# Kernel tuning notes

Hardware: AMD Instinct MI355X
Metric: run time of the kernel (lower is better)

Reference implementation:

```python
import jax, jax.numpy as jnp
import numpy as np

N_NODES = 100000
N_EDGES = 1600000
NODE_DIM = 128
EDGE_DIM = 64
MSG_DIM = 128
NODE_DIM_OUT = 128


def setup_inputs() -> dict:
    key = jax.random.key(0)
    k1, k2, k3, k4, k5, k6, k7 = jax.random.split(key, 7)
    node_emb = jax.random.normal(k1, (N_NODES, NODE_DIM), dtype=jnp.float32)
    edge_index = jax.random.randint(k2, (2, N_EDGES), 0, N_NODES, dtype=jnp.int64)
    edge_emb = jax.random.normal(k3, (N_EDGES, EDGE_DIM), dtype=jnp.float32)
    # Linear params (stored as [in, out]; torch uses [out, in] with x @ W.T)
    s_msg = 1.0 / np.sqrt(NODE_DIM + EDGE_DIM)
    W_msg = jax.random.uniform(k4, (NODE_DIM + EDGE_DIM, MSG_DIM), jnp.float32, -s_msg, s_msg)
    b_msg = jax.random.uniform(k5, (MSG_DIM,), jnp.float32, -s_msg, s_msg)
    s_upd = 1.0 / np.sqrt(NODE_DIM + MSG_DIM)
    W_upd = jax.random.uniform(k6, (NODE_DIM + MSG_DIM, NODE_DIM_OUT), jnp.float32, -s_upd, s_upd)
    b_upd = jax.random.uniform(k7, (NODE_DIM_OUT,), jnp.float32, -s_upd, s_upd)
    return {"node_emb": node_emb, "edge_index": edge_index, "edge_emb": edge_emb,
            "W_msg": W_msg, "b_msg": b_msg, "W_upd": W_upd, "b_upd": b_upd}


def reference(node_emb, edge_index, edge_emb, W_msg, b_msg, W_upd, b_upd):
    # PyG MessagePassing default flow: x_j = x[edge_index[0]] (source),
    # messages aggregated (mean) at edge_index[1] (target).
    src = edge_index[0]
    dst = edge_index[1]
    n = node_emb.shape[0]

    x_j = node_emb[src]                                    # [E, node_dim] gather
    msg_in = jnp.concatenate([x_j, edge_emb], axis=1)      # [E, node_dim+edge_dim]
    msg = jax.nn.relu(msg_in @ W_msg + b_msg)              # [E, msg_dim]

    # scatter-mean aggregate to nodes
    summed = jax.ops.segment_sum(msg, dst, num_segments=n)  # [N, msg_dim]
    counts = jax.ops.segment_sum(jnp.ones((msg.shape[0],), dtype=msg.dtype), dst, num_segments=n)
    mean_msg = summed / jnp.maximum(counts, 1.0)[:, None]

    upd_in = jnp.concatenate([node_emb, mean_msg], axis=1)  # [N, node_dim+msg_dim]
    h = jax.nn.relu(upd_in @ W_upd + b_upd)                 # [N, node_dim_out]
    # dropout is identity in eval mode; normalize=False (default)
    return h
```

## Files before the change

### kernel.cpp

```cpp
#include <hip/hip_runtime.h>
#include <hip/hip_bf16.h>

#define N_NODES 100000
#define N_EDGES 1600000
#define D_NODE 128
#define D_EDGE 64
#define D_MSG 128
#define K1 192
#define K2 256
#define D_OUT 128
#define NSB 98
#define TILE 64
#define NT (N_EDGES / TILE)

using frag8 = __attribute__((ext_vector_type(8))) short;
using facc  = __attribute__((ext_vector_type(4))) float;
typedef int   i32x4 __attribute__((ext_vector_type(4)));
typedef float f32x2 __attribute__((ext_vector_type(2)));

static __device__ __forceinline__ unsigned short f2bf(float f) {
    unsigned int u = __float_as_uint(f);
    u = u + 0x7fffu + ((u >> 16) & 1u);
    return (unsigned short)(u >> 16);
}
static __device__ __forceinline__ float bflo(unsigned int u) { return __uint_as_float(u << 16); }
static __device__ __forceinline__ float bfhi(unsigned int u) { return __uint_as_float(u & 0xffff0000u); }

union F8 { unsigned short s[8]; frag8 f; uint4 u4; };

static __device__ __forceinline__ frag8 pack8(float4 a, float4 b) {
    F8 u;
    u.s[0] = f2bf(a.x); u.s[1] = f2bf(a.y); u.s[2] = f2bf(a.z); u.s[3] = f2bf(a.w);
    u.s[4] = f2bf(b.x); u.s[5] = f2bf(b.y); u.s[6] = f2bf(b.z); u.s[7] = f2bf(b.w);
    return u.f;
}

__global__ void prep_all_kernel(const float* __restrict__ Wm, const float* __restrict__ Wu,
                                const float* __restrict__ node_emb, const int* __restrict__ dst,
                                unsigned short* __restrict__ WtM, unsigned short* __restrict__ WtU,
                                unsigned int* __restrict__ nodeB32, int* __restrict__ cnt) {
    int idx0 = blockIdx.x * blockDim.x + threadIdx.x;
    int stride = gridDim.x * blockDim.x;
    for (int idx = idx0; idx < 128 * K1; idx += stride) {
        int o = idx / K1, k = idx - o * K1;
        WtM[idx] = f2bf(Wm[k * D_MSG + o]);
    }
    for (int idx = idx0; idx < 128 * K2; idx += stride) {
        int o = idx >> 8, k = idx & 255;
        WtU[idx] = f2bf(Wu[k * D_OUT + o]);
    }
    const int total = N_NODES * 64;
    for (int i = idx0; i < total; i += stride) {
        float2 v = *(const float2*)&node_emb[(size_t)i * 2];
        nodeB32[i] = (unsigned)f2bf(v.x) | ((unsigned)f2bf(v.y) << 16);
    }
    for (int e = idx0; e < N_EDGES; e += stride) {
        int d = min(max(dst[e], 0), N_NODES - 1);
        atomicAdd(&cnt[d], 1);
    }
}

__global__ __launch_bounds__(1024) void scan_blocks(const int* __restrict__ cnt,
                                                    int* __restrict__ base,
                                                    int* __restrict__ part) {
    __shared__ int sh[1024];
    int i = blockIdx.x * 1024 + threadIdx.x;
    int c = (i < N_NODES) ? cnt[i] : 0;
    sh[threadIdx.x] = c;
    __syncthreads();
    for (int s = 1; s < 1024; s <<= 1) {
        int t = (threadIdx.x >= s) ? sh[threadIdx.x - s] : 0;
        __syncthreads();
        sh[threadIdx.x] += t;
        __syncthreads();
    }
    if (i < N_NODES) base[i] = sh[threadIdx.x] - c;
    if (threadIdx.x == 1023) part[blockIdx.x] = sh[1023];
}

__global__ __launch_bounds__(1024) void scan_add(int* __restrict__ base, const int* __restrict__ part) {
    __shared__ int soff;
    if (threadIdx.x < 64) {
        int l = threadIdx.x;
        int v = 0;
        if (l < blockIdx.x) v += part[l];
        if (l + 64 < blockIdx.x) v += part[l + 64];
#pragma unroll
        for (int s = 32; s; s >>= 1) v += __shfl_down(v, s, 64);
        if (l == 0) soff = v;
    }
    __syncthreads();
    int i = blockIdx.x * 1024 + threadIdx.x;
    if (i < N_NODES) base[i] += soff;
}

__global__ void scatter_kernel(const int* __restrict__ dst, const int* __restrict__ src,
                               const int* __restrict__ base, int* __restrict__ cursor,
                               i32x4* __restrict__ meta) {
    int idx0 = blockIdx.x * blockDim.x + threadIdx.x;
    int stride = gridDim.x * blockDim.x;
    for (int e = idx0; e < N_EDGES; e += stride) {
        int d = min(max(dst[e], 0), N_NODES - 1);
        int pos = base[d] + atomicAdd(&cursor[d], 1);
        i32x4 m; m[0] = e; m[1] = src[e]; m[2] = d; m[3] = 0;
        __builtin_nontemporal_store(m, &meta[pos]);
    }
}

__global__ __launch_bounds__(256, 4) void msg_fused_kernel(
    const unsigned short* __restrict__ nodeB, const i32x4* __restrict__ meta,
    const float* __restrict__ edge_emb, const unsigned short* __restrict__ WtM,
    const float* __restrict__ b_msg, const int* __restrict__ base,
    const int* __restrict__ cnt, unsigned int* __restrict__ meanB32,
    float* __restrict__ spill)
{
    __shared__ unsigned short sIn[TILE][192];
    __shared__ unsigned short sMsg[TILE][128];

    const int lane = threadIdx.x & 63;
    const int wav  = threadIdx.x >> 6;
    const int j = lane & 15;
    const int q = lane >> 4;

    frag8 wfr[2][6];
#pragma unroll
    for (int m2 = 0; m2 < 2; ++m2) {
        const unsigned short* wrow = WtM + ((wav * 2 + m2) * 16 + j) * K1;
#pragma unroll
        for (int kc = 0; kc < 6; ++kc)
            wfr[m2][kc] = *(const frag8*)&wrow[(kc * 4 + q) * 8];
    }
    float bias[2][4];
#pragma unroll
    for (int m2 = 0; m2 < 2; ++m2)
#pragma unroll
        for (int r = 0; r < 4; ++r) bias[m2][r] = b_msg[(wav * 2 + m2) * 16 + q * 4 + r];

    const int eL = threadIdx.x >> 2;
    const int qt = threadIdx.x & 3;
    const int swz = eL & 7;

    uint4  nst[4];
    float4 est[4];

    const int t0 = blockIdx.x;

    {
        const int e = t0 * TILE + eL;
        const i32x4 m = meta[e];
        const int sp = min(max(m[1], 0), N_NODES - 1);
        const unsigned short* nrow = nodeB + (size_t)sp * D_NODE + qt * 32;
#pragma unroll
        for (int i = 0; i < 4; ++i) nst[i] = *(const uint4*)&nrow[i * 8];
        const float* erow = edge_emb + (size_t)m[0] * D_EDGE + qt * 16;
#pragma unroll
        for (int i = 0; i < 4; ++i) est[i] = *(const float4*)&erow[i * 4];
    }

#pragma unroll 1
    for (int t = t0; t < NT; t += gridDim.x) {
        const int e0 = t * TILE;

        __syncthreads();

        {
            unsigned short* drow = &sIn[eL][0];
#pragma unroll
            for (int i = 0; i < 4; ++i)
                *(uint4*)&drow[((4 * qt + i) ^ swz) * 8] = nst[i];
#pragma unroll
            for (int h = 0; h < 2; ++h) {
                F8 u;
                u.f = pack8(est[h * 2], est[h * 2 + 1]);
                *(uint4*)&drow[((16 + 2 * qt + h) ^ swz) * 8] = u.u4;
            }
        }
        __syncthreads();

        const int tn = t + gridDim.x;
        if (tn < NT) {
            const int e = tn * TILE + eL;
            const i32x4 m = meta[e];
            const int sp = min(max(m[1], 0), N_NODES - 1);
            const unsigned short* nrow = nodeB + (size_t)sp * D_NODE + qt * 32;
#pragma unroll
            for (int i = 0; i < 4; ++i) nst[i] = *(const uint4*)&nrow[i * 8];
            const float* erow = edge_emb + (size_t)m[0] * D_EDGE + qt * 16;
#pragma unroll
            for (int i = 0; i < 4; ++i) est[i] = *(const float4*)&erow[i * 4];
        }

        facc acc[2][4];
#pragma unroll
        for (int m2 = 0; m2 < 2; ++m2)
#pragma unroll
            for (int eg = 0; eg < 4; ++eg) { facc z = {0.f,0.f,0.f,0.f}; acc[m2][eg] = z; }

        const int rsw = j & 7;
#pragma unroll
        for (int eg = 0; eg < 4; ++eg) {
            const unsigned short* irow = &sIn[eg * 16 + j][0];
#pragma unroll
            for (int kc = 0; kc < 6; ++kc) {
                frag8 b = *(const frag8*)&irow[((4 * kc + q) ^ rsw) * 8];
                acc[0][eg] = __builtin_amdgcn_mfma_f32_16x16x32_bf16(wfr[0][kc], b, acc[0][eg], 0, 0, 0);
                acc[1][eg] = __builtin_amdgcn_mfma_f32_16x16x32_bf16(wfr[1][kc], b, acc[1][eg], 0, 0, 0);
            }
        }

#pragma unroll
        for (int eg = 0; eg < 4; ++eg) {
            unsigned short* mrow = &sMsg[eg * 16 + j][0];
#pragma unroll
            for (int m2 = 0; m2 < 2; ++m2) {
                float v0 = fmaxf(acc[m2][eg][0] + bias[m2][0], 0.f);
                float v1 = fmaxf(acc[m2][eg][1] + bias[m2][1], 0.f);
                float v2 = fmaxf(acc[m2][eg][2] + bias[m2][2], 0.f);
                float v3 = fmaxf(acc[m2][eg][3] + bias[m2][3], 0.f);
                uint2 w;
                w.x = (unsigned)f2bf(v0) | ((unsigned)f2bf(v1) << 16);
                w.y = (unsigned)f2bf(v2) | ((unsigned)f2bf(v3) << 16);
                int c64 = wav * 8 + m2 * 4 + q;
                *(uint2*)&mrow[(c64 ^ rsw) * 4] = w;
            }
        }
        __syncthreads();

        const int d_lo = ((const int*)&meta[e0])[2];
        const int d_hi = ((const int*)&meta[e0 + TILE - 1])[2];
        for (int n = d_lo + wav; n <= d_hi; n += 4) {
            const int b = base[n];
            const int c = cnt[n];
            const int lo = max(b - e0, 0);
            const int hi = min(b + c - e0, TILE);
            float s0 = 0.f, s1 = 0.f;
            for (int r = lo; r < hi; ++r) {
                const unsigned* mr = (const unsigned*)&sMsg[r][0];
                unsigned u = mr[(((lane >> 1) ^ (r & 7)) << 1) | (lane & 1)];
                s0 += bflo(u); s1 += bfhi(u);
            }
            const float inv = 1.0f / fmaxf((float)c, 1.0f);
            s0 *= inv; s1 *= inv;
            if (b >= e0 && b + c <= e0 + TILE) {
                unsigned int w = (unsigned)f2bf(s0) | ((unsigned)f2bf(s1) << 16);
                __builtin_nontemporal_store(w, &meanB32[(size_t)n * 64 + lane]);
            } else {
                int slot = (n == d_lo) ? 0 : 1;
                f32x2 w; w[0] = s0; w[1] = s1;
                __builtin_nontemporal_store(
                    w, (f32x2*)(spill + ((size_t)(t * 2 + slot)) * D_MSG + lane * 2));
            }
        }
    }
}

__global__ __launch_bounds__(256) void cleanup_kernel(
    const i32x4* __restrict__ meta, const int* __restrict__ base,
    const int* __restrict__ cnt, const float* __restrict__ spill,
    unsigned int* __restrict__ meanB32)
{
    const int wav = threadIdx.x >> 6;
    const int lane = threadIdx.x & 63;
    const int nstride = gridDim.x * 4;
    for (int n = blockIdx.x * 4 + wav; n < N_NODES; n += nstride) {
        const int c = cnt[n];
        float s0 = 0.f, s1 = 0.f;
        if (c > 0) {
            const int b = base[n];
            const int t0 = b >> 6, t1 = (b + c - 1) >> 6;
            if (t0 == t1) continue;
            for (int t = t0; t <= t1; ++t) {
                const int slot = (((const int*)&meta[t * TILE])[2] == n) ? 0 : 1;
                const float* sp = spill + ((size_t)(t * 2 + slot)) * D_MSG + lane * 2;
                s0 += sp[0]; s1 += sp[1];
            }
        }
        meanB32[(size_t)n * 64 + lane] = (unsigned)f2bf(s0) | ((unsigned)f2bf(s1) << 16);
    }
}

__global__ __launch_bounds__(256) void node_gemm_kernel(
    const unsigned short* __restrict__ nodeB, const unsigned short* __restrict__ meanB,
    const unsigned short* __restrict__ WtU, const float* __restrict__ b_upd,
    float* __restrict__ out)
{
    __shared__ unsigned short sW[128 * K2];

    for (int idx = threadIdx.x; idx < 128 * 32; idx += 256) {
        int o = idx >> 5, ch = idx & 31;
        *(uint4*)&sW[o * K2 + (ch ^ (o & 7)) * 8] = *(const uint4*)&WtU[o * K2 + ch * 8];
    }

    const int lane = threadIdx.x & 63;
    const int wav  = threadIdx.x >> 6;
    const int j = lane & 15;
    const int q = lane >> 4;
    const int rs = j & 7;

    float bias[32];
#pragma unroll
    for (int mt = 0; mt < 8; ++mt)
#pragma unroll
        for (int r = 0; r < 4; ++r) bias[mt * 4 + r] = b_upd[mt * 16 + q * 4 + r];
    __syncthreads();

    const int n0w = blockIdx.x * 128 + wav * 32;

#pragma unroll 1
    for (int g = 0; g < 2; ++g) {
        const int n = n0w + g * 16 + j;
        const bool valid = (n < N_NODES);
        const size_t nn = valid ? (size_t)n : 0;

        frag8 bfr[8];
        const unsigned short* nrow = nodeB + nn * D_NODE;
#pragma unroll
        for (int kc = 0; kc < 4; ++kc)
            bfr[kc] = *(const frag8*)&nrow[kc * 32 + q * 8];
        const unsigned short* mrow = meanB + nn * D_MSG;
#pragma unroll
        for (int kc = 0; kc < 4; ++kc)
            bfr[4 + kc] = *(const frag8*)&mrow[kc * 32 + q * 8];

        facc acc[8];
#pragma unroll
        for (int mt = 0; mt < 8; ++mt) { facc z = {0.f, 0.f, 0.f, 0.f}; acc[mt] = z; }

#pragma unroll
        for (int mt = 0; mt < 8; ++mt) {
            const unsigned short* wrow = &sW[(mt * 16 + j) * K2];
#pragma unroll
            for (int kc = 0; kc < 8; ++kc) {
                frag8 a = *(const frag8*)&wrow[((kc * 4 + q) ^ rs) * 8];
                acc[mt] = __builtin_amdgcn_mfma_f32_16x16x32_bf16(a, bfr[kc], acc[mt], 0, 0, 0);
            }
        }

        if (valid) {
            float* orow = out + (size_t)n * D_OUT;
#pragma unroll
            for (int mt = 0; mt < 8; ++mt)
#pragma unroll
                for (int r = 0; r < 4; ++r)
                    orow[mt * 16 + q * 4 + r] = fmaxf(acc[mt][r] + bias[mt * 4 + r], 0.f);
        }
    }
}

__global__ void prep_w_kernel(const float* __restrict__ Wm, const float* __restrict__ Wu,
                              unsigned short* __restrict__ WtM, unsigned short* __restrict__ WtU) {
    int idx0 = blockIdx.x * blockDim.x + threadIdx.x;
    int stride = gridDim.x * blockDim.x;
    for (int idx = idx0; idx < 128 * K1; idx += stride) {
        int o = idx / K1, k = idx - o * K1;
        WtM[idx] = f2bf(Wm[k * D_MSG + o]);
    }
    for (int idx = idx0; idx < 128 * K2; idx += stride) {
        int o = idx >> 8, k = idx & 255;
        WtU[idx] = f2bf(Wu[k * D_OUT + o]);
    }
}

__global__ void hist_kernel(const int* __restrict__ dst, int* __restrict__ cnt) {
    int idx0 = blockIdx.x * blockDim.x + threadIdx.x;
    int stride = gridDim.x * blockDim.x;
    for (int e = idx0; e < N_EDGES; e += stride) {
        int d = min(max(dst[e], 0), N_NODES - 1);
        atomicAdd(&cnt[d], 1);
    }
}

__global__ __launch_bounds__(256) void msg_agg_kernel_fb(
    const float* __restrict__ node_emb, const i32x4* __restrict__ meta,
    const float* __restrict__ edge_emb, const unsigned short* __restrict__ WtM,
    const float* __restrict__ b_msg, const int* __restrict__ cnt,
    float* __restrict__ mean)
{
    __shared__ unsigned short sW[128 * K1];

    for (int idx = threadIdx.x; idx < 128 * 24; idx += 256) {
        int o = idx / 24, ch = idx % 24;
        *(uint4*)&sW[o * K1 + (ch ^ (o & 7)) * 8] = *(const uint4*)&WtM[o * K1 + ch * 8];
    }

    const int lane = threadIdx.x & 63;
    const int wav  = threadIdx.x >> 6;
    const int j = lane & 15;
    const int q = lane >> 4;

    float bias[32];
#pragma unroll
    for (int mt = 0; mt < 8; ++mt)
#pragma unroll
        for (int r = 0; r < 4; ++r) bias[mt * 4 + r] = b_msg[mt * 16 + q * 4 + r];
    __syncthreads();

    const int e0w = blockIdx.x * 256 + wav * 64;
    float carry[32];
    int carry_d = -1;

#pragma unroll 1
    for (int g = 0; g < 4; ++g) {
        const int e = e0w + g * 16 + j;
        const i32x4 m = meta[e];
        const int p = m[0];
        const int d = m[2];
        const int sp = min(max(m[1], 0), N_NODES - 1);
        const float invc = 1.0f / (float)cnt[d];

        frag8 bfr[6];
        const float* nrow = node_emb + (size_t)sp * D_NODE;
#pragma unroll
        for (int kc = 0; kc < 4; ++kc) {
            float4 a = *(const float4*)&nrow[kc * 32 + q * 8];
            float4 c = *(const float4*)&nrow[kc * 32 + q * 8 + 4];
            bfr[kc] = pack8(a, c);
        }
        const float* erow = edge_emb + (size_t)p * D_EDGE;
#pragma unroll
        for (int kc = 0; kc < 2; ++kc) {
            float4 a = *(const float4*)&erow[kc * 32 + q * 8];
            float4 c = *(const float4*)&erow[kc * 32 + q * 8 + 4];
            bfr[4 + kc] = pack8(a, c);
        }

        facc acc[8];
#pragma unroll
        for (int mt = 0; mt < 8; ++mt) { facc z = {0.f, 0.f, 0.f, 0.f}; acc[mt] = z; }

#pragma unroll
        for (int mt = 0; mt < 8; ++mt) {
            const unsigned short* wrow = &sW[(mt * 16 + j) * K1];
            const int rs = j & 7;
#pragma unroll
            for (int kc = 0; kc < 6; ++kc) {
                frag8 a = *(const frag8*)&wrow[((kc * 4 + q) ^ rs) * 8];
                acc[mt] = __builtin_amdgcn_mfma_f32_16x16x32_bf16(a, bfr[kc], acc[mt], 0, 0, 0);
            }
        }

        float v[32];
#pragma unroll
        for (int mt = 0; mt < 8; ++mt)
#pragma unroll
            for (int r = 0; r < 4; ++r) {
                float t = acc[mt][r] + bias[mt * 4 + r];
                v[mt * 4 + r] = fmaxf(t, 0.f) * invc;
            }

        int dprev = __shfl_up(d, 1, 16);
        int head = (j == 0 || d != dprev) ? 1 : 0;
        int seg = head;
#pragma unroll
        for (int s = 1; s < 16; s <<= 1) { int t = __shfl_up(seg, s, 16); if (j >= s) seg += t; }
        int sg1 = __shfl_up(seg, 1, 16);
        int sg2 = __shfl_up(seg, 2, 16);
        int sg4 = __shfl_up(seg, 4, 16);
        int sg8 = __shfl_up(seg, 8, 16);
        bool ok1 = (j >= 1) && (sg1 == seg);
        bool ok2 = (j >= 2) && (sg2 == seg);
        bool ok4 = (j >= 4) && (sg4 == seg);
        bool ok8 = (j >= 8) && (sg8 == seg);

#pragma unroll
        for (int i = 0; i < 32; ++i) { float t = __shfl_up(v[i], 1, 16); if (ok1) v[i] += t; }
#pragma unroll
        for (int i = 0; i < 32; ++i) { float t = __shfl_up(v[i], 2, 16); if (ok2) v[i] += t; }
#pragma unroll
        for (int i = 0; i < 32; ++i) { float t = __shfl_up(v[i], 4, 16); if (ok4) v[i] += t; }
#pragma unroll
        for (int i = 0; i < 32; ++i) { float t = __shfl_up(v[i], 8, 16); if (ok8) v[i] += t; }

        int d0 = __shfl(d, 0, 16);
        if (g > 0) {
            if (d0 != carry_d) {
                if (j == 0) {
                    float* mrow = mean + (size_t)carry_d * D_MSG;
#pragma unroll
                    for (int mt = 0; mt < 8; ++mt)
#pragma unroll
                        for (int r = 0; r < 4; ++r)
                            atomicAdd(&mrow[mt * 16 + q * 4 + r], carry[mt * 4 + r]);
                }
            } else if (seg == 1) {
#pragma unroll
                for (int i = 0; i < 32; ++i) v[i] += carry[i];
            }
        }

#pragma unroll
        for (int i = 0; i < 32; ++i) carry[i] = __shfl(v[i], 15, 16);
        carry_d = __shfl(d, 15, 16);

        int dnext = __shfl_down(d, 1, 16);
        bool tail = (j < 15) ? (dnext != d) : (g == 3);
        if (tail) {
            float* mrow = mean + (size_t)d * D_MSG;
#pragma unroll
            for (int mt = 0; mt < 8; ++mt)
#pragma unroll
                for (int r = 0; r < 4; ++r)
                    atomicAdd(&mrow[mt * 16 + q * 4 + r], v[mt * 4 + r]);
        }
    }
}

__global__ __launch_bounds__(256) void node_kernel_fb(
    const float* __restrict__ node_emb, const float* __restrict__ mean,
    const unsigned short* __restrict__ WtU, const float* __restrict__ b_upd,
    float* __restrict__ out)
{
    __shared__ unsigned short sW[128 * K2];

    for (int idx = threadIdx.x; idx < 128 * 32; idx += 256) {
        int o = idx >> 5, ch = idx & 31;
        *(uint4*)&sW[o * K2 + (ch ^ (o & 7)) * 8] = *(const uint4*)&WtU[o * K2 + ch * 8];
    }

    const int lane = threadIdx.x & 63;
    const int wav  = threadIdx.x >> 6;
    const int j = lane & 15;
    const int q = lane >> 4;

    float bias[32];
#pragma unroll
    for (int mt = 0; mt < 8; ++mt)
#pragma unroll
        for (int r = 0; r < 4; ++r) bias[mt * 4 + r] = b_upd[mt * 16 + q * 4 + r];
    __syncthreads();

    const int n0w = blockIdx.x * 256 + wav * 64;

#pragma unroll 1
    for (int g = 0; g < 4; ++g) {
        const int n = n0w + g * 16 + j;
        const bool valid = (n < N_NODES);
        const size_t nn = valid ? (size_t)n : 0;

        frag8 bfr[8];
        const float* nrow = node_emb + nn * D_NODE;
#pragma unroll
        for (int kc = 0; kc < 4; ++kc) {
            float4 a = *(const float4*)&nrow[kc * 32 + q * 8];
            float4 c = *(const float4*)&nrow[kc * 32 + q * 8 + 4];
            bfr[kc] = pack8(a, c);
        }
        const float* mrow = mean + nn * D_MSG;
#pragma unroll
        for (int kc = 0; kc < 4; ++kc) {
            float4 a = *(const float4*)&mrow[kc * 32 + q * 8];
            float4 c = *(const float4*)&mrow[kc * 32 + q * 8 + 4];
            bfr[4 + kc] = pack8(a, c);
        }

        facc acc[8];
#pragma unroll
        for (int mt = 0; mt < 8; ++mt) { facc z = {0.f, 0.f, 0.f, 0.f}; acc[mt] = z; }

#pragma unroll
        for (int mt = 0; mt < 8; ++mt) {
            const unsigned short* wrow = &sW[(mt * 16 + j) * K2];
            const int rs = j & 7;
#pragma unroll
            for (int kc = 0; kc < 8; ++kc) {
                frag8 a = *(const frag8*)&wrow[((kc * 4 + q) ^ rs) * 8];
                acc[mt] = __builtin_amdgcn_mfma_f32_16x16x32_bf16(a, bfr[kc], acc[mt], 0, 0, 0);
            }
        }

        if (valid) {
            float* orow = out + (size_t)n * D_OUT;
#pragma unroll
            for (int mt = 0; mt < 8; ++mt)
#pragma unroll
                for (int r = 0; r < 4; ++r)
                    orow[mt * 16 + q * 4 + r] = fmaxf(acc[mt][r] + bias[mt * 4 + r], 0.f);
        }
    }
}

extern "C" void kernel_launch(void* const* d_in, const int* in_sizes, int n_in,
                              void* d_out, int out_size, void* d_ws, size_t ws_size,
                              hipStream_t stream) {
    const float* node_emb = (const float*)d_in[0];
    const int*   edge_idx = (const int*)d_in[1];
    const float* edge_emb = (const float*)d_in[2];
    const float* W_msg    = (const float*)d_in[3];
    const float* b_msg    = (const float*)d_in[4];
    const float* W_upd    = (const float*)d_in[5];
    const float* b_upd    = (const float*)d_in[6];
    float* out = (float*)d_out;

    const int* src = edge_idx;
    const int* dst = edge_idx + N_EDGES;

    char* W = (char*)d_ws;

    if (ws_size >= 104000000ULL) {
        unsigned short* meanB = (unsigned short*)(W + 0);
        int* cnt     = (int*)(W + 25600000);
        int* cursor  = (int*)(W + 26000000);
        int* base    = (int*)(W + 26400000);
        int* part    = (int*)(W + 26800000);
        i32x4* meta  = (i32x4*)(W + 26800512);
        unsigned short* WtM   = (unsigned short*)(W + 52400512);
        unsigned short* WtU   = (unsigned short*)(W + 52449664);
        unsigned short* nodeB = (unsigned short*)(W + 52515200);
        float* spill = (float*)(W + 78115200);

        hipMemsetAsync(W + 25600000, 0, 800000, stream);

        prep_all_kernel<<<2048, 256, 0, stream>>>(W_msg, W_upd, node_emb, dst,
                                                  WtM, WtU, (unsigned int*)nodeB, cnt);
        scan_blocks<<<NSB, 1024, 0, stream>>>(cnt, base, part);
        scan_add<<<NSB, 1024, 0, stream>>>(base, part);
        scatter_kernel<<<1024, 256, 0, stream>>>(dst, src, base, cursor, meta);
        msg_fused_kernel<<<2048, 256, 0, stream>>>(nodeB, meta, edge_emb,
                                                   WtM, b_msg, base, cnt,
                                                   (unsigned int*)meanB, spill);
        cleanup_kernel<<<1600, 256, 0, stream>>>(meta, base, cnt, spill,
                                                 (unsigned int*)meanB);
        node_gemm_kernel<<<782, 256, 0, stream>>>(nodeB, meanB, WtU, b_upd, out);
    } else {
        float* mean  = (float*)W;
        int* cnt     = (int*)(W + 51200000);
        int* cursor  = (int*)(W + 51600000);
        int* base    = (int*)(W + 52000000);
        int* part    = (int*)(W + 52400000);
        i32x4* meta  = (i32x4*)(W + 52400512);
        unsigned short* WtM = (unsigned short*)(W + 78000512);
        unsigned short* WtU = (unsigned short*)(W + 78049664);

        hipMemsetAsync(d_ws, 0, 52000000, stream);

        prep_w_kernel<<<224, 256, 0, stream>>>(W_msg, W_upd, WtM, WtU);
        hist_kernel<<<1024, 256, 0, stream>>>(dst, cnt);
        scan_blocks<<<NSB, 1024, 0, stream>>>(cnt, base, part);
        scan_add<<<NSB, 1024, 0, stream>>>(base, part);
        scatter_kernel<<<1024, 256, 0, stream>>>(dst, src, base, cursor, meta);
        msg_agg_kernel_fb<<<6250, 256, 0, stream>>>(node_emb, meta, edge_emb, WtM,
                                                    b_msg, cnt, mean);
        node_kernel_fb<<<391, 256, 0, stream>>>(node_emb, mean, WtU, b_upd, out);
    }
}
```

Before: 588.8 us.

## Widen node conversion loads, vectorize output stores, relax msg kernel occupancy

The node embedding bf16 conversion now handles four floats per thread with float4 loads and uint2 stores. The node GEMM output is written as 16-byte nontemporal vector stores, and the spill reads in cleanup use nontemporal float2 loads. The message kernel's launch bounds drop the minimum-blocks hint from 4 to 3, which lets it use more registers at the cost of occupancy. These changes aim to cut memory instruction count and cache pollution, but the occupancy change could help or hurt the dominant message kernel.

```diff
diff --git a/kernel.cpp b/kernel.cpp
--- a/kernel.cpp
+++ b/kernel.cpp
@@ -17,6 +17,7 @@
 using facc  = __attribute__((ext_vector_type(4))) float;
 typedef int   i32x4 __attribute__((ext_vector_type(4)));
 typedef float f32x2 __attribute__((ext_vector_type(2)));
+typedef float f32x4v __attribute__((ext_vector_type(4)));
 
 static __device__ __forceinline__ unsigned short f2bf(float f) {
     unsigned int u = __float_as_uint(f);
@@ -37,8 +38,8 @@
 
 __global__ void prep_all_kernel(const float* __restrict__ Wm, const float* __restrict__ Wu,
                                 const float* __restrict__ node_emb, const int* __restrict__ dst,
-                                unsigned short* __restrict__ WtM, unsigned short* __restrict__ WtU,
-                                unsigned int* __restrict__ nodeB32, int* __restrict__ cnt) {
+                                unsigned int* __restrict__ nodeB32, int* __restrict__ cnt,
+                                unsigned short* __restrict__ WtM, unsigned short* __restrict__ WtU) {
     int idx0 = blockIdx.x * blockDim.x + threadIdx.x;
     int stride = gridDim.x * blockDim.x;
     for (int idx = idx0; idx < 128 * K1; idx += stride) {
@@ -49,10 +50,13 @@
         int o = idx >> 8, k = idx & 255;
         WtU[idx] = f2bf(Wu[k * D_OUT + o]);
     }
-    const int total = N_NODES * 64;
+    const int total = N_NODES * 32;
     for (int i = idx0; i < total; i += stride) {
-        float2 v = *(const float2*)&node_emb[(size_t)i * 2];
-        nodeB32[i] = (unsigned)f2bf(v.x) | ((unsigned)f2bf(v.y) << 16);
+        float4 v = *(const float4*)&node_emb[(size_t)i * 4];
+        uint2 w;
+        w.x = (unsigned)f2bf(v.x) | ((unsigned)f2bf(v.y) << 16);
+        w.y = (unsigned)f2bf(v.z) | ((unsigned)f2bf(v.w) << 16);
+        *(uint2*)&nodeB32[(size_t)i * 2] = w;
     }
     for (int e = idx0; e < N_EDGES; e += stride) {
         int d = min(max(dst[e], 0), N_NODES - 1);
@@ -107,7 +111,7 @@
     }
 }
 
-__global__ __launch_bounds__(256, 4) void msg_fused_kernel(
+__global__ __launch_bounds__(256, 3) void msg_fused_kernel(
     const unsigned short* __restrict__ nodeB, const i32x4* __restrict__ meta,
     const float* __restrict__ edge_emb, const unsigned short* __restrict__ WtM,
     const float* __restrict__ b_msg, const int* __restrict__ base,
@@ -271,8 +275,9 @@
             if (t0 == t1) continue;
             for (int t = t0; t <= t1; ++t) {
                 const int slot = (((const int*)&meta[t * TILE])[2] == n) ? 0 : 1;
-                const float* sp = spill + ((size_t)(t * 2 + slot)) * D_MSG + lane * 2;
-                s0 += sp[0]; s1 += sp[1];
+                f32x2 v = __builtin_nontemporal_load(
+                    (const f32x2*)(spill + ((size_t)(t * 2 + slot)) * D_MSG + lane * 2));
+                s0 += v[0]; s1 += v[1];
             }
         }
         meanB32[(size_t)n * 64 + lane] = (unsigned)f2bf(s0) | ((unsigned)f2bf(s1) << 16);
@@ -339,10 +344,14 @@
         if (valid) {
             float* orow = out + (size_t)n * D_OUT;
 #pragma unroll
-            for (int mt = 0; mt < 8; ++mt)
-#pragma unroll
-                for (int r = 0; r < 4; ++r)
-                    orow[mt * 16 + q * 4 + r] = fmaxf(acc[mt][r] + bias[mt * 4 + r], 0.f);
+            for (int mt = 0; mt < 8; ++mt) {
+                f32x4v w;
+                w[0] = fmaxf(acc[mt][0] + bias[mt * 4 + 0], 0.f);
+                w[1] = fmaxf(acc[mt][1] + bias[mt * 4 + 1], 0.f);
+                w[2] = fmaxf(acc[mt][2] + bias[mt * 4 + 2], 0.f);
+                w[3] = fmaxf(acc[mt][3] + bias[mt * 4 + 3], 0.f);
+                __builtin_nontemporal_store(w, (f32x4v*)&orow[mt * 16 + q * 4]);
+            }
         }
     }
 }
@@ -611,7 +620,7 @@
         hipMemsetAsync(W + 25600000, 0, 800000, stream);
 
         prep_all_kernel<<<2048, 256, 0, stream>>>(W_msg, W_upd, node_emb, dst,
-                                                  WtM, WtU, (unsigned int*)nodeB, cnt);
+                                                  (unsigned int*)nodeB, cnt, WtM, WtU);
         scan_blocks<<<NSB, 1024, 0, stream>>>(cnt, base, part);
         scan_add<<<NSB, 1024, 0, stream>>>(base, part);
         scatter_kernel<<<1024, 256, 0, stream>>>(dst, src, base, cursor, meta);
```

Result: faster. 570.9 us (-3.0%).
